# Performance work log

Measured on AMD Instinct MI355X. Metric: run time of the kernel, lower is better.

The kernel has to match this reference:

```python
import jax, jax.numpy as jnp
import numpy as np

D_MODEL = 1024
NUM_HEADS = 16
D_K = D_MODEL // NUM_HEADS
B, T = 2, 2048


def setup_inputs() -> dict:
    key = jax.random.key(0)
    ks = jax.random.split(key, 9)
    s = 1.0 / np.sqrt(D_MODEL)
    inp = {"x": jax.random.normal(ks[0], (B, T, D_MODEL), dtype=jnp.float32)}
    for i, name in enumerate(["q", "k", "v", "out"]):
        inp[f"W_{name}"] = jax.random.uniform(ks[1 + 2 * i], (D_MODEL, D_MODEL), jnp.float32, -s, s)
        inp[f"b_{name}"] = jax.random.uniform(ks[2 + 2 * i], (D_MODEL,), jnp.float32, -s, s)
    return inp


def reference(x, W_q, b_q, W_k, b_k, W_v, b_v, W_out, b_out):
    b, t, _ = x.shape
    # torch Linear: y = x @ W.T + b
    def proj(inp, W, bias):
        y = inp @ W.T + bias
        return y.reshape(b, -1, NUM_HEADS, D_K).transpose(0, 2, 1, 3)  # [B,H,T,d_k]

    Q = proj(x, W_q, b_q)
    K = proj(x, W_k, b_k)
    V = proj(x, W_v, b_v)
    scores = jnp.einsum("bhqd,bhkd->bhqk", Q, K) / jnp.sqrt(jnp.float32(D_K))
    attn = jax.nn.softmax(scores, axis=-1)
    ctx = jnp.einsum("bhqk,bhkd->bhqd", attn, V)
    ctx = ctx.transpose(0, 2, 1, 3).reshape(b, t, D_MODEL)
    return ctx @ W_out.T + b_out
```

## Files before the change

kernel.cpp:

```cpp
#include <hip/hip_runtime.h>
#include <hip/hip_bf16.h>

typedef __attribute__((ext_vector_type(8))) short short8;
typedef __attribute__((ext_vector_type(4))) short short4v;
typedef __attribute__((ext_vector_type(4))) float floatx4;

__device__ __forceinline__ unsigned short f2b(float f) {
  unsigned int v;
  __builtin_memcpy(&v, &f, 4);
  unsigned int r = (v + 0x7FFFu + ((v >> 16) & 1u)) >> 16;
  return (unsigned short)r;
}

__device__ __forceinline__ unsigned int f2b_pk(float a, float b) {
#if __has_builtin(__builtin_amdgcn_cvt_pk_bf16_f32)
  typedef __attribute__((ext_vector_type(2))) __bf16 bf16x2;
  bf16x2 r = __builtin_amdgcn_cvt_pk_bf16_f32(a, b);
  unsigned int u;
  __builtin_memcpy(&u, &r, 4);
  return u;
#else
  return ((unsigned int)f2b(b) << 16) | (unsigned int)f2b(a);
#endif
}

__device__ __forceinline__ float fast_exp2(float x) {
#if __has_builtin(__builtin_amdgcn_exp2f)
  return __builtin_amdgcn_exp2f(x);
#else
  return __builtin_exp2f(x);
#endif
}

__device__ __forceinline__ void async_copy16(const void* g, void* l) {
  __builtin_amdgcn_global_load_lds(
      (const __attribute__((address_space(1))) unsigned int*)g,
      (__attribute__((address_space(3))) unsigned int*)l, 16, 0, 0);
}

#define QSCALE 0.18033688011112042f

__global__ __launch_bounds__(256) void cvt_all_kernel(
    const float* __restrict__ x,
    const float* __restrict__ w0, const float* __restrict__ w1,
    const float* __restrict__ w2, const float* __restrict__ w3,
    unsigned short* __restrict__ xb,
    unsigned short* __restrict__ d0, unsigned short* __restrict__ d1,
    unsigned short* __restrict__ d2, unsigned short* __restrict__ d3)
{
  int gid = blockIdx.x * 256 + threadIdx.x;
  const float* src;
  unsigned short* dst;
  size_t off;
  if (gid < (1 << 20)) {
    src = x; dst = xb; off = gid;
  } else {
    int g = gid - (1 << 20);
    int w = g >> 18;
    off = g & 0x3FFFF;
    src = (w == 0) ? w0 : (w == 1) ? w1 : (w == 2) ? w2 : w3;
    dst = (w == 0) ? d0 : (w == 1) ? d1 : (w == 2) ? d2 : d3;
  }
  floatx4 v = *(const floatx4*)(src + off * 4);
  unsigned int lo = f2b_pk(v[0], v[1]), hi = f2b_pk(v[2], v[3]);
  unsigned long long r = ((unsigned long long)hi << 32) | lo;
  *(unsigned long long*)(dst + off * 4) = r;
}

__global__ __launch_bounds__(256) void gemm_qkv_kernel(
    const unsigned short* __restrict__ A,
    const unsigned short* __restrict__ W0, const unsigned short* __restrict__ W1,
    const unsigned short* __restrict__ W2,
    const float* __restrict__ bias0, const float* __restrict__ bias1,
    const float* __restrict__ bias2,
    unsigned short* __restrict__ Qo, unsigned short* __restrict__ Ko,
    unsigned short* __restrict__ VTo)
{
  const int z = blockIdx.z;
  const unsigned short* W  = (z == 0) ? W0 : (z == 1) ? W1 : W2;
  const float* bias        = (z == 0) ? bias0 : (z == 1) ? bias1 : bias2;

  __shared__ alignas(16) unsigned short sA[128 * 64];
  __shared__ alignas(16) unsigned short sB[128 * 64];

  const int tid  = threadIdx.x;
  const int lane = tid & 63;
  const int wave = tid >> 6;
  const int col  = lane & 15;
  const int quad = lane >> 4;
  const int wm   = (wave >> 1) * 64;
  const int wn   = (wave & 1) * 64;
  const int m0   = blockIdx.y * 128;
  const int n0   = blockIdx.x * 128;
  const int c7   = col & 7;

  floatx4 acc[4][4];
#pragma unroll
  for (int i = 0; i < 4; ++i)
#pragma unroll
    for (int j = 0; j < 4; ++j) acc[i][j] = (floatx4){0.f, 0.f, 0.f, 0.f};

  for (int k0 = 0; k0 < 1024; k0 += 64) {
    __syncthreads();
#pragma unroll
    for (int i = 0; i < 4; ++i) {
      int c   = i * 256 + tid;
      int row = c >> 3;
      int ko  = ((c & 7) ^ (row & 7)) * 8;
      async_copy16(A + (size_t)(m0 + row) * 1024 + k0 + ko, sA + c * 8);
      async_copy16(W + (size_t)(n0 + row) * 1024 + k0 + ko, sB + c * 8);
    }
    __syncthreads();
#pragma unroll
    for (int ks = 0; ks < 2; ++ks) {
      const int rp = ((ks * 4 + quad) ^ c7) * 8;
      short8 af[4], bf[4];
#pragma unroll
      for (int mi = 0; mi < 4; ++mi)
        af[mi] = *(const short8*)(sA + (wm + mi * 16 + col) * 64 + rp);
#pragma unroll
      for (int ni = 0; ni < 4; ++ni)
        bf[ni] = *(const short8*)(sB + (wn + ni * 16 + col) * 64 + rp);
#pragma unroll
      for (int mi = 0; mi < 4; ++mi)
#pragma unroll
        for (int ni = 0; ni < 4; ++ni)
          acc[mi][ni] = __builtin_amdgcn_mfma_f32_16x16x32_bf16(af[mi], bf[ni], acc[mi][ni], 0, 0, 0);
    }
  }

#pragma unroll
  for (int ni = 0; ni < 4; ++ni) {
    int n = n0 + wn + ni * 16 + col;
    float bv = bias[n];
#pragma unroll
    for (int mi = 0; mi < 4; ++mi) {
      int mbase = m0 + wm + mi * 16 + quad * 4;
      if (z == 2) {
        int d = n & 63, h = n >> 6;
        int bb = mbase >> 11, t = mbase & 2047;
        unsigned int lo = f2b_pk(acc[mi][ni][0] + bv, acc[mi][ni][1] + bv);
        unsigned int hi = f2b_pk(acc[mi][ni][2] + bv, acc[mi][ni][3] + bv);
        unsigned long long wv = ((unsigned long long)hi << 32) | lo;
        *(unsigned long long*)(VTo + (((size_t)bb * 16 + h) * 64 + d) * 2048 + t) = wv;
      } else {
#pragma unroll
        for (int r = 0; r < 4; ++r) {
          int m = mbase + r;
          float val = acc[mi][ni][r] + bv;
          if (z == 0) Qo[(size_t)m * 1024 + n] = f2b(val * QSCALE);
          else        Ko[(size_t)m * 1024 + n] = f2b(val);
        }
      }
    }
  }
}

__global__ __launch_bounds__(256) void gemm_out_kernel(
    const unsigned short* __restrict__ A, const unsigned short* __restrict__ W,
    const float* __restrict__ bias, float* __restrict__ DF)
{
  __shared__ alignas(16) unsigned short sA[128 * 64];
  __shared__ alignas(16) unsigned short sB[64 * 64];

  const int tid  = threadIdx.x;
  const int lane = tid & 63;
  const int wave = tid >> 6;
  const int col  = lane & 15;
  const int quad = lane >> 4;
  const int wm   = (wave >> 1) * 64;
  const int wn   = (wave & 1) * 32;
  const int m0   = blockIdx.y * 128;
  const int n0   = blockIdx.x * 64;
  const int c7   = col & 7;

  floatx4 acc[4][2];
#pragma unroll
  for (int i = 0; i < 4; ++i)
#pragma unroll
    for (int j = 0; j < 2; ++j) acc[i][j] = (floatx4){0.f, 0.f, 0.f, 0.f};

  for (int k0 = 0; k0 < 1024; k0 += 64) {
    __syncthreads();
#pragma unroll
    for (int i = 0; i < 4; ++i) {
      int c   = i * 256 + tid;
      int row = c >> 3;
      int ko  = ((c & 7) ^ (row & 7)) * 8;
      async_copy16(A + (size_t)(m0 + row) * 1024 + k0 + ko, sA + c * 8);
    }
#pragma unroll
    for (int i = 0; i < 2; ++i) {
      int c   = i * 256 + tid;
      int row = c >> 3;
      int ko  = ((c & 7) ^ (row & 7)) * 8;
      async_copy16(W + (size_t)(n0 + row) * 1024 + k0 + ko, sB + c * 8);
    }
    __syncthreads();
#pragma unroll
    for (int ks = 0; ks < 2; ++ks) {
      const int rp = ((ks * 4 + quad) ^ c7) * 8;
      short8 af[4], bf[2];
#pragma unroll
      for (int mi = 0; mi < 4; ++mi)
        af[mi] = *(const short8*)(sA + (wm + mi * 16 + col) * 64 + rp);
#pragma unroll
      for (int ni = 0; ni < 2; ++ni)
        bf[ni] = *(const short8*)(sB + (wn + ni * 16 + col) * 64 + rp);
#pragma unroll
      for (int mi = 0; mi < 4; ++mi)
#pragma unroll
        for (int ni = 0; ni < 2; ++ni)
          acc[mi][ni] = __builtin_amdgcn_mfma_f32_16x16x32_bf16(af[mi], bf[ni], acc[mi][ni], 0, 0, 0);
    }
  }

#pragma unroll
  for (int ni = 0; ni < 2; ++ni) {
    int n = n0 + wn + ni * 16 + col;
    float bv = bias[n];
#pragma unroll
    for (int mi = 0; mi < 4; ++mi) {
      int mbase = m0 + wm + mi * 16 + quad * 4;
#pragma unroll
      for (int r = 0; r < 4; ++r)
        DF[(size_t)(mbase + r) * 1024 + n] = acc[mi][ni][r] + bv;
    }
  }
}

__global__ __launch_bounds__(256, 4) void attention_kernel(
    const unsigned short* __restrict__ Q, const unsigned short* __restrict__ K,
    const unsigned short* __restrict__ VT, unsigned short* __restrict__ CTX)
{
  __shared__ alignas(16) unsigned short sK[2][4096];
  __shared__ alignas(16) unsigned short sV[2][4096];
  __shared__ alignas(16) unsigned short sP[4][16 * 64];

  const int flat = blockIdx.x;
  const int idx  = flat >> 3;
  const int bh   = (flat & 7) * 4 + (idx >> 5);
  const int q0   = (idx & 31) * 64;
  const int b = bh >> 4, h = bh & 15;

  const int tid  = threadIdx.x;
  const int lane = tid & 63;
  const int wave = tid >> 6;
  const int col  = lane & 15;
  const int quad = lane >> 4;
  const int c7   = col & 7;
  const int swz8 = (quad ^ ((col >> 1) & 3)) * 8;

  const int srow = tid >> 2;
  const int sko  = ((tid & 3) ^ ((tid >> 3) & 3)) * 8;

  const unsigned short* kbase = K + ((size_t)b * 2048 + srow) * 1024 + h * 64;
  const unsigned short* vbase = VT + ((size_t)bh * 64 + srow) * 2048;

  short8 qf[2];
  {
    const unsigned short* qp =
        Q + ((size_t)(b * 2048 + q0 + wave * 16 + col)) * 1024 + h * 64 + quad * 8;
    qf[0] = *(const short8*)qp;
    qf[1] = *(const short8*)(qp + 32);
  }

#pragma unroll
  for (int i = 0; i < 2; ++i) {
    async_copy16(kbase + i * 32 + sko, sK[0] + (i * 256 + tid) * 8);
    async_copy16(vbase + i * 32 + sko, sV[0] + (i * 256 + tid) * 8);
  }

  floatx4 Oacc[4];
#pragma unroll
  for (int f = 0; f < 4; ++f) Oacc[f] = (floatx4){0.f, 0.f, 0.f, 0.f};
  float lacc = 0.f;

  unsigned short* myP = &sP[wave][0];

#pragma unroll 2
  for (int kt = 0; kt < 2048; kt += 64) {
    const int cur = (kt >> 6) & 1;
    const unsigned short* sKc = sK[cur];
    const unsigned short* sVc = sV[cur];
    __syncthreads();
    if (kt + 64 < 2048) {
      const int nxt = cur ^ 1;
#pragma unroll
      for (int i = 0; i < 2; ++i) {
        async_copy16(kbase + (size_t)(kt + 64) * 1024 + i * 32 + sko,
                     sK[nxt] + (i * 256 + tid) * 8);
        async_copy16(vbase + (kt + 64) + i * 32 + sko,
                     sV[nxt] + (i * 256 + tid) * 8);
      }
    }

    floatx4 ST[4];
#pragma unroll
    for (int f = 0; f < 4; ++f) {
      ST[f] = (floatx4){0.f, 0.f, 0.f, 0.f};
      short8 kf0 = *(const short8*)(sKc + (f * 16 + col) * 32 + swz8);
      ST[f] = __builtin_amdgcn_mfma_f32_16x16x32_bf16(kf0, qf[0], ST[f], 0, 0, 0);
      short8 kf1 = *(const short8*)(sKc + 2048 + (f * 16 + col) * 32 + swz8);
      ST[f] = __builtin_amdgcn_mfma_f32_16x16x32_bf16(kf1, qf[1], ST[f], 0, 0, 0);
    }

#pragma unroll
    for (int f = 0; f < 4; ++f) {
      float p0 = fast_exp2(ST[f][0]);
      float p1 = fast_exp2(ST[f][1]);
      float p2 = fast_exp2(ST[f][2]);
      float p3 = fast_exp2(ST[f][3]);
      lacc += (p0 + p1) + (p2 + p3);
      unsigned long long w =
          ((unsigned long long)f2b_pk(p2, p3) << 32) | f2b_pk(p0, p1);
      *(unsigned long long*)(myP + col * 64 +
                             (((f * 2 + (quad >> 1)) ^ c7) * 8) + (quad & 1) * 4) = w;
    }

    short8 pf0 = *(const short8*)(myP + col * 64 + ((quad ^ c7) * 8));
    short8 pf1 = *(const short8*)(myP + col * 64 + (((quad + 4) ^ c7) * 8));
#pragma unroll
    for (int f = 0; f < 4; ++f) {
      short8 vf0 = *(const short8*)(sVc + (f * 16 + col) * 32 + swz8);
      Oacc[f] = __builtin_amdgcn_mfma_f32_16x16x32_bf16(pf0, vf0, Oacc[f], 0, 0, 0);
      short8 vf1 = *(const short8*)(sVc + 2048 + (f * 16 + col) * 32 + swz8);
      Oacc[f] = __builtin_amdgcn_mfma_f32_16x16x32_bf16(pf1, vf1, Oacc[f], 0, 0, 0);
    }
  }

  lacc += __shfl_xor(lacc, 16, 64);
  lacc += __shfl_xor(lacc, 32, 64);
  float inv[4];
#pragma unroll
  for (int r = 0; r < 4; ++r) inv[r] = 1.f / __shfl(lacc, quad * 4 + r, 16);

#pragma unroll
  for (int f = 0; f < 4; ++f) {
#pragma unroll
    for (int r = 0; r < 4; ++r) {
      int q = q0 + wave * 16 + quad * 4 + r;
      int d = f * 16 + col;
      CTX[(size_t)(b * 2048 + q) * 1024 + h * 64 + d] = f2b(Oacc[f][r] * inv[r]);
    }
  }
}

extern "C" void kernel_launch(void* const* d_in, const int* in_sizes, int n_in,
                              void* d_out, int out_size, void* d_ws, size_t ws_size,
                              hipStream_t stream) {
  const float* x   = (const float*)d_in[0];
  const float* W_q = (const float*)d_in[1];
  const float* b_q = (const float*)d_in[2];
  const float* W_k = (const float*)d_in[3];
  const float* b_k = (const float*)d_in[4];
  const float* W_v = (const float*)d_in[5];
  const float* b_v = (const float*)d_in[6];
  const float* W_o = (const float*)d_in[7];
  const float* b_o = (const float*)d_in[8];
  float* out = (float*)d_out;

  const size_t NX = (size_t)4096 * 1024;
  const size_t NW = (size_t)1024 * 1024;

  unsigned short* p   = (unsigned short*)d_ws;
  unsigned short* xb  = p;  p += NX;
  unsigned short* Wqb = p;  p += NW;
  unsigned short* Wkb = p;  p += NW;
  unsigned short* Wvb = p;  p += NW;
  unsigned short* Wob = p;  p += NW;
  unsigned short* Q   = p;  p += NX;
  unsigned short* Kb  = p;  p += NX;
  unsigned short* VT  = p;  p += NX;
  unsigned short* CTX = p;  p += NX;

  dim3 blk(256);
  cvt_all_kernel<<<dim3(8192), blk, 0, stream>>>(
      x, W_q, W_k, W_v, W_o, xb, Wqb, Wkb, Wvb, Wob);
  gemm_qkv_kernel<<<dim3(8, 32, 3), blk, 0, stream>>>(
      xb, Wqb, Wkb, Wvb, b_q, b_k, b_v, Q, Kb, VT);
  attention_kernel<<<dim3(1024), blk, 0, stream>>>(Q, Kb, VT, CTX);
  gemm_out_kernel<<<dim3(16, 32), blk, 0, stream>>>(CTX, Wob, b_o, out);
}
```

Measured before the change: 207.5 us.

## Process 32 query rows per wave in attention to reuse K/V fragments

Each wave of the attention kernel now handles two 16-row query subtiles (128 queries per block instead of 64), so every K and V fragment read from LDS feeds two MFMAs. The grid is halved to 512 blocks and the P scratch buffer is doubled. This cuts LDS traffic and global K/V reloads per query, but it raises register pressure (launch bounds lowered to 2 blocks per SIMD) and may leave some compute units underfilled.

```diff
diff --git a/kernel.cpp b/kernel.cpp
--- a/kernel.cpp
+++ b/kernel.cpp
@@ -229,18 +229,18 @@
   }
 }
 
-__global__ __launch_bounds__(256, 4) void attention_kernel(
+__global__ __launch_bounds__(256, 2) void attention_kernel(
     const unsigned short* __restrict__ Q, const unsigned short* __restrict__ K,
     const unsigned short* __restrict__ VT, unsigned short* __restrict__ CTX)
 {
   __shared__ alignas(16) unsigned short sK[2][4096];
   __shared__ alignas(16) unsigned short sV[2][4096];
-  __shared__ alignas(16) unsigned short sP[4][16 * 64];
+  __shared__ alignas(16) unsigned short sP[4][32 * 64];
 
   const int flat = blockIdx.x;
   const int idx  = flat >> 3;
-  const int bh   = (flat & 7) * 4 + (idx >> 5);
-  const int q0   = (idx & 31) * 64;
+  const int bh   = (flat & 7) * 4 + (idx >> 4);
+  const int q0   = (idx & 15) * 128;
   const int b = bh >> 4, h = bh & 15;
 
   const int tid  = threadIdx.x;
@@ -257,12 +257,14 @@
   const unsigned short* kbase = K + ((size_t)b * 2048 + srow) * 1024 + h * 64;
   const unsigned short* vbase = VT + ((size_t)bh * 64 + srow) * 2048;
 
-  short8 qf[2];
+  short8 qfA[2], qfB[2];
   {
     const unsigned short* qp =
-        Q + ((size_t)(b * 2048 + q0 + wave * 16 + col)) * 1024 + h * 64 + quad * 8;
-    qf[0] = *(const short8*)qp;
-    qf[1] = *(const short8*)(qp + 32);
+        Q + ((size_t)(b * 2048 + q0 + wave * 32 + col)) * 1024 + h * 64 + quad * 8;
+    qfA[0] = *(const short8*)qp;
+    qfA[1] = *(const short8*)(qp + 32);
+    qfB[0] = *(const short8*)(qp + 16 * 1024);
+    qfB[1] = *(const short8*)(qp + 16 * 1024 + 32);
   }
 
 #pragma unroll
@@ -271,10 +273,13 @@
     async_copy16(vbase + i * 32 + sko, sV[0] + (i * 256 + tid) * 8);
   }
 
-  floatx4 Oacc[4];
-#pragma unroll
-  for (int f = 0; f < 4; ++f) Oacc[f] = (floatx4){0.f, 0.f, 0.f, 0.f};
-  float lacc = 0.f;
+  floatx4 OA[4], OB[4];
+#pragma unroll
+  for (int f = 0; f < 4; ++f) {
+    OA[f] = (floatx4){0.f, 0.f, 0.f, 0.f};
+    OB[f] = (floatx4){0.f, 0.f, 0.f, 0.f};
+  }
+  float laccA = 0.f, laccB = 0.f;
 
   unsigned short* myP = &sP[wave][0];
 
@@ -295,53 +300,75 @@
       }
     }
 
-    floatx4 ST[4];
+    floatx4 STA[4], STB[4];
 #pragma unroll
     for (int f = 0; f < 4; ++f) {
-      ST[f] = (floatx4){0.f, 0.f, 0.f, 0.f};
       short8 kf0 = *(const short8*)(sKc + (f * 16 + col) * 32 + swz8);
-      ST[f] = __builtin_amdgcn_mfma_f32_16x16x32_bf16(kf0, qf[0], ST[f], 0, 0, 0);
       short8 kf1 = *(const short8*)(sKc + 2048 + (f * 16 + col) * 32 + swz8);
-      ST[f] = __builtin_amdgcn_mfma_f32_16x16x32_bf16(kf1, qf[1], ST[f], 0, 0, 0);
+      STA[f] = (floatx4){0.f, 0.f, 0.f, 0.f};
+      STA[f] = __builtin_amdgcn_mfma_f32_16x16x32_bf16(kf0, qfA[0], STA[f], 0, 0, 0);
+      STA[f] = __builtin_amdgcn_mfma_f32_16x16x32_bf16(kf1, qfA[1], STA[f], 0, 0, 0);
+      STB[f] = (floatx4){0.f, 0.f, 0.f, 0.f};
+      STB[f] = __builtin_amdgcn_mfma_f32_16x16x32_bf16(kf0, qfB[0], STB[f], 0, 0, 0);
+      STB[f] = __builtin_amdgcn_mfma_f32_16x16x32_bf16(kf1, qfB[1], STB[f], 0, 0, 0);
     }
 
 #pragma unroll
     for (int f = 0; f < 4; ++f) {
-      float p0 = fast_exp2(ST[f][0]);
-      float p1 = fast_exp2(ST[f][1]);
-      float p2 = fast_exp2(ST[f][2]);
-      float p3 = fast_exp2(ST[f][3]);
-      lacc += (p0 + p1) + (p2 + p3);
-      unsigned long long w =
-          ((unsigned long long)f2b_pk(p2, p3) << 32) | f2b_pk(p0, p1);
+      float a0 = fast_exp2(STA[f][0]);
+      float a1 = fast_exp2(STA[f][1]);
+      float a2 = fast_exp2(STA[f][2]);
+      float a3 = fast_exp2(STA[f][3]);
+      laccA += (a0 + a1) + (a2 + a3);
+      unsigned long long wA =
+          ((unsigned long long)f2b_pk(a2, a3) << 32) | f2b_pk(a0, a1);
       *(unsigned long long*)(myP + col * 64 +
-                             (((f * 2 + (quad >> 1)) ^ c7) * 8) + (quad & 1) * 4) = w;
-    }
-
-    short8 pf0 = *(const short8*)(myP + col * 64 + ((quad ^ c7) * 8));
-    short8 pf1 = *(const short8*)(myP + col * 64 + (((quad + 4) ^ c7) * 8));
+                             (((f * 2 + (quad >> 1)) ^ c7) * 8) + (quad & 1) * 4) = wA;
+      float b0 = fast_exp2(STB[f][0]);
+      float b1 = fast_exp2(STB[f][1]);
+      float b2 = fast_exp2(STB[f][2]);
+      float b3 = fast_exp2(STB[f][3]);
+      laccB += (b0 + b1) + (b2 + b3);
+      unsigned long long wB =
+          ((unsigned long long)f2b_pk(b2, b3) << 32) | f2b_pk(b0, b1);
+      *(unsigned long long*)(myP + (16 + col) * 64 +
+                             (((f * 2 + (quad >> 1)) ^ c7) * 8) + (quad & 1) * 4) = wB;
+    }
+
+    short8 pfA0 = *(const short8*)(myP + col * 64 + ((quad ^ c7) * 8));
+    short8 pfA1 = *(const short8*)(myP + col * 64 + (((quad + 4) ^ c7) * 8));
+    short8 pfB0 = *(const short8*)(myP + (16 + col) * 64 + ((quad ^ c7) * 8));
+    short8 pfB1 = *(const short8*)(myP + (16 + col) * 64 + (((quad + 4) ^ c7) * 8));
 #pragma unroll
     for (int f = 0; f < 4; ++f) {
       short8 vf0 = *(const short8*)(sVc + (f * 16 + col) * 32 + swz8);
-      Oacc[f] = __builtin_amdgcn_mfma_f32_16x16x32_bf16(pf0, vf0, Oacc[f], 0, 0, 0);
       short8 vf1 = *(const short8*)(sVc + 2048 + (f * 16 + col) * 32 + swz8);
-      Oacc[f] = __builtin_amdgcn_mfma_f32_16x16x32_bf16(pf1, vf1, Oacc[f], 0, 0, 0);
-    }
-  }
-
-  lacc += __shfl_xor(lacc, 16, 64);
-  lacc += __shfl_xor(lacc, 32, 64);
-  float inv[4];
-#pragma unroll
-  for (int r = 0; r < 4; ++r) inv[r] = 1.f / __shfl(lacc, quad * 4 + r, 16);
+      OA[f] = __builtin_amdgcn_mfma_f32_16x16x32_bf16(pfA0, vf0, OA[f], 0, 0, 0);
+      OA[f] = __builtin_amdgcn_mfma_f32_16x16x32_bf16(pfA1, vf1, OA[f], 0, 0, 0);
+      OB[f] = __builtin_amdgcn_mfma_f32_16x16x32_bf16(pfB0, vf0, OB[f], 0, 0, 0);
+      OB[f] = __builtin_amdgcn_mfma_f32_16x16x32_bf16(pfB1, vf1, OB[f], 0, 0, 0);
+    }
+  }
+
+  laccA += __shfl_xor(laccA, 16, 64);
+  laccA += __shfl_xor(laccA, 32, 64);
+  laccB += __shfl_xor(laccB, 16, 64);
+  laccB += __shfl_xor(laccB, 32, 64);
+  float invA[4], invB[4];
+#pragma unroll
+  for (int r = 0; r < 4; ++r) {
+    invA[r] = 1.f / __shfl(laccA, quad * 4 + r, 16);
+    invB[r] = 1.f / __shfl(laccB, quad * 4 + r, 16);
+  }
 
 #pragma unroll
   for (int f = 0; f < 4; ++f) {
 #pragma unroll
     for (int r = 0; r < 4; ++r) {
-      int q = q0 + wave * 16 + quad * 4 + r;
+      int qA = q0 + wave * 32 + quad * 4 + r;
       int d = f * 16 + col;
-      CTX[(size_t)(b * 2048 + q) * 1024 + h * 64 + d] = f2b(Oacc[f][r] * inv[r]);
+      CTX[(size_t)(b * 2048 + qA) * 1024 + h * 64 + d] = f2b(OA[f][r] * invA[r]);
+      CTX[(size_t)(b * 2048 + qA + 16) * 1024 + h * 64 + d] = f2b(OB[f][r] * invB[r]);
     }
   }
 }
@@ -379,6 +406,6 @@
       x, W_q, W_k, W_v, W_o, xb, Wqb, Wkb, Wvb, Wob);
   gemm_qkv_kernel<<<dim3(8, 32, 3), blk, 0, stream>>>(
       xb, Wqb, Wkb, Wvb, b_q, b_k, b_v, Q, Kb, VT);
-  attention_kernel<<<dim3(1024), blk, 0, stream>>>(Q, Kb, VT, CTX);
+  attention_kernel<<<dim3(512), blk, 0, stream>>>(Q, Kb, VT, CTX);
   gemm_out_kernel<<<dim3(16, 32), blk, 0, stream>>>(CTX, Wob, b_o, out);
 }
```

Measured after the change: 206.8 us. No clear change (-0.3%).
